# Optimization experiments

Hardware: AMD Instinct MI355X
Metric: run time of the kernel (lower is better)

## Reference

```python
import jax, jax.numpy as jnp
import numpy as np

VOCAB, EMB, H, NL = 50257, 1024, 2048, 2


def _lstm_cell(x, h, c, Wih, Whh, bih, bhh):
    # x: [1, in], h/c: [1, H]; PyTorch gate order i, f, g, o
    gates = x @ Wih.T + bih + h @ Whh.T + bhh  # [1, 4H]
    i, f, g, o = jnp.split(gates, 4, axis=-1)
    c2 = jax.nn.sigmoid(f) * c + jax.nn.sigmoid(i) * jnp.tanh(g)
    h2 = jax.nn.sigmoid(o) * jnp.tanh(c2)
    return h2, c2


def setup_inputs() -> dict:
    key = jax.random.key(0)
    ks = jax.random.split(key, 12)
    s = 0.02  # keep gate pre-activations in a sane range
    return {
        "input_ids": jax.random.randint(ks[0], (1,), 0, VOCAB, dtype=jnp.int64),
        "h0": jax.random.normal(ks[1], (2 * NL, 1, H), jnp.float32) * 0.1,
        "c0": jax.random.normal(ks[2], (2 * NL, 1, H), jnp.float32) * 0.1,
        "emb": jax.random.normal(ks[3], (VOCAB, EMB), jnp.float32),
        "W_ih_l0": jax.random.normal(ks[4], (2, 4 * H, EMB), jnp.float32) * s,
        "W_hh_l0": jax.random.normal(ks[5], (2, 4 * H, H), jnp.float32) * s,
        "b_ih_l0": jax.random.normal(ks[6], (2, 4 * H), jnp.float32) * s,
        "b_hh_l0": jax.random.normal(ks[7], (2, 4 * H), jnp.float32) * s,
        "W_ih_l1": jax.random.normal(ks[8], (2, 4 * H, 2 * H), jnp.float32) * s,
        "W_hh_l1": jax.random.normal(ks[9], (2, 4 * H, H), jnp.float32) * s,
        "b_ih_l1": jax.random.normal(ks[10], (2, 4 * H), jnp.float32) * s,
        "b_hh_l1": jax.random.normal(ks[11], (2, 4 * H), jnp.float32) * s,
    }


def reference(input_ids, h0, c0, emb, W_ih_l0, W_hh_l0, b_ih_l0, b_hh_l0,
              W_ih_l1, W_hh_l1, b_ih_l1, b_hh_l1):
    # embedded = embedding(input).view(1, 1, -1) -> seq_len=1, batch=1
    x = emb[input_ids]  # [1, EMB]
    layers = [(W_ih_l0, W_hh_l0, b_ih_l0, b_hh_l0),
              (W_ih_l1, W_hh_l1, b_ih_l1, b_hh_l1)]
    h_out, c_out = [], []
    for l, (Wih, Whh, bih, bhh) in enumerate(layers):
        # seq_len == 1: fwd and bwd directions both see the single timestep
        hf, cf = _lstm_cell(x, h0[2 * l], c0[2 * l], Wih[0], Whh[0], bih[0], bhh[0])
        hb, cb = _lstm_cell(x, h0[2 * l + 1], c0[2 * l + 1], Wih[1], Whh[1], bih[1], bhh[1])
        h_out += [hf, hb]
        c_out += [cf, cb]
        x = jnp.concatenate([hf, hb], axis=-1)  # [1, 2H] input to next layer
    output = x[None]  # [1, 1, 2H] (seq, batch, 2*hidden)
    h_n = jnp.stack(h_out, axis=0)  # [2*NL, 1, H]
    c_n = jnp.stack(c_out, axis=0)
    return output, h_n, c_n
```

## Files before the change

kernel.cpp:

```cpp
#include <hip/hip_runtime.h>


#define HID 2048
#define G4H 8192

__device__ __forceinline__ float wave_reduce_sum(float v) {
    #pragma unroll
    for (int off = 32; off > 0; off >>= 1)
        v += __shfl_down(v, off, 64);
    return v;
}
__device__ __forceinline__ float sigmoidf_(float v) { return 1.f / (1.f + expf(-v)); }

__global__ __launch_bounds__(256) void k1_gates0_part1(
    const int*   __restrict__ tok,
    const float* __restrict__ emb,
    const float* __restrict__ Wih0,
    const float* __restrict__ Whh0,
    const float* __restrict__ bih0,
    const float* __restrict__ bhh0,
    const float* __restrict__ Whh1,
    const float* __restrict__ bih1,
    const float* __restrict__ bhh1,
    const float* __restrict__ h0,
    float* __restrict__ gates0,
    float* __restrict__ part1)
{
    const int wave = (int)((blockIdx.x * blockDim.x + threadIdx.x) >> 6);
    const int lane = (int)(threadIdx.x & 63);

    if (wave < 2 * G4H) {
        const int dir = wave >> 13;
        const int r   = wave & (G4H - 1);
        const float*  x   = emb + (size_t)tok[0] * 1024;
        const float4* wih = (const float4*)(Wih0 + ((size_t)dir * G4H + r) * 1024);
        const float4* whh = (const float4*)(Whh0 + ((size_t)dir * G4H + r) * HID);
        const float4* xv  = (const float4*)x;
        const float4* hv  = (const float4*)(h0 + (size_t)dir * HID);

        float acc = 0.f;
        #pragma unroll
        for (int i = 0; i < 1024 / 4 / 64; ++i) {
            float4 w = wih[lane + i * 64], b = xv[lane + i * 64];
            acc += w.x * b.x + w.y * b.y + w.z * b.z + w.w * b.w;
        }
        #pragma unroll
        for (int i = 0; i < HID / 4 / 64; ++i) {
            float4 w = whh[lane + i * 64], b = hv[lane + i * 64];
            acc += w.x * b.x + w.y * b.y + w.z * b.z + w.w * b.w;
        }
        acc = wave_reduce_sum(acc);
        if (lane == 0) {
            int row = dir * G4H + r;
            gates0[row] = acc + bih0[row] + bhh0[row];
        }
    } else {
        const int w2  = wave - 2 * G4H;
        const int dir = w2 >> 13;
        const int r   = w2 & (G4H - 1);
        const float4* whh = (const float4*)(Whh1 + ((size_t)dir * G4H + r) * HID);
        const float4* hv  = (const float4*)(h0 + (size_t)(2 + dir) * HID);

        float acc = 0.f;
        #pragma unroll
        for (int i = 0; i < HID / 4 / 64; ++i) {
            float4 w = whh[lane + i * 64], b = hv[lane + i * 64];
            acc += w.x * b.x + w.y * b.y + w.z * b.z + w.w * b.w;
        }
        acc = wave_reduce_sum(acc);
        if (lane == 0) {
            int row = dir * G4H + r;
            part1[row] = acc + bih1[row] + bhh1[row];
        }
    }
}

__global__ __launch_bounds__(256) void k2_layer1(
    const float* __restrict__ gates0,
    const float* __restrict__ part1,
    const float* __restrict__ Wih1,
    const float* __restrict__ c0,
    float* __restrict__ out)
{
    __shared__ float x1[2 * HID];

    #pragma unroll
    for (int k = 0; k < 16; ++k) {
        const int idx = k * 256 + (int)threadIdx.x;
        const int dir = idx >> 11;
        const int j   = idx & (HID - 1);
        const float* g = gates0 + dir * G4H;
        float gi = g[j];
        float gf = g[HID + j];
        float gg = g[2 * HID + j];
        float go = g[3 * HID + j];
        float cp = c0[(size_t)dir * HID + j];
        float c2 = sigmoidf_(gf) * cp + sigmoidf_(gi) * tanhf(gg);
        float h2 = sigmoidf_(go) * tanhf(c2);
        x1[idx] = h2;
        if (blockIdx.x == 0) {
            out[4096  + (size_t)dir * HID + j] = h2;
            out[12288 + (size_t)dir * HID + j] = c2;
        }
    }
    __syncthreads();

    const int wave = (int)((blockIdx.x * blockDim.x + threadIdx.x) >> 6);
    const int lane = (int)(threadIdx.x & 63);
    const int dir  = wave >> 11;
    const int j    = wave & (HID - 1);

    const float4* xv = (const float4*)x1;
    float acc[4] = {0.f, 0.f, 0.f, 0.f};
    #pragma unroll
    for (int g = 0; g < 4; ++g) {
        const float4* wih = (const float4*)(Wih1 + ((size_t)dir * G4H + g * HID + j) * 4096);
        #pragma unroll 4
        for (int i = 0; i < 4096 / 4 / 64; ++i) {
            float4 w = wih[lane + i * 64], b = xv[lane + i * 64];
            acc[g] += w.x * b.x + w.y * b.y + w.z * b.z + w.w * b.w;
        }
    }
    #pragma unroll
    for (int g = 0; g < 4; ++g) acc[g] = wave_reduce_sum(acc[g]);

    if (lane == 0) {
        const int rb = dir * G4H + j;
        float gi = acc[0] + part1[rb];
        float gf = acc[1] + part1[rb + HID];
        float gg = acc[2] + part1[rb + 2 * HID];
        float go = acc[3] + part1[rb + 3 * HID];
        float cp = c0[(size_t)(2 + dir) * HID + j];
        float c2 = sigmoidf_(gf) * cp + sigmoidf_(gi) * tanhf(gg);
        float h2 = sigmoidf_(go) * tanhf(c2);
        out[4096  + (size_t)(2 + dir) * HID + j] = h2;
        out[12288 + (size_t)(2 + dir) * HID + j] = c2;
        out[(size_t)dir * HID + j] = h2;
    }
}

extern "C" void kernel_launch(void* const* d_in, const int* in_sizes, int n_in,
                              void* d_out, int out_size, void* d_ws, size_t ws_size,
                              hipStream_t stream) {
    const int*   ids  = (const int*)  d_in[0];
    const float* h0   = (const float*)d_in[1];
    const float* c0   = (const float*)d_in[2];
    const float* emb  = (const float*)d_in[3];
    const float* Wih0 = (const float*)d_in[4];
    const float* Whh0 = (const float*)d_in[5];
    const float* bih0 = (const float*)d_in[6];
    const float* bhh0 = (const float*)d_in[7];
    const float* Wih1 = (const float*)d_in[8];
    const float* Whh1 = (const float*)d_in[9];
    const float* bih1 = (const float*)d_in[10];
    const float* bhh1 = (const float*)d_in[11];

    float* out    = (float*)d_out;
    float* gates0 = (float*)d_ws;
    float* part1  = gates0 + 2 * G4H;

    k1_gates0_part1<<<8192, 256, 0, stream>>>(ids, emb, Wih0, Whh0, bih0, bhh0,
                                              Whh1, bih1, bhh1, h0, gates0, part1);
    k2_layer1<<<1024, 256, 0, stream>>>(gates0, part1, Wih1, c0, out);
}
```

Measured before the change: 116.9 us.

## Fuse layer-0 cell into gate GEMV kernel and split layer-1 gates across waves

The layer-0 LSTM cell nonlinearity moves into the first kernel. Each block now computes the four gate rows of one hidden unit in four waves, combines them through shared memory, and writes h/c directly. This removes the redundant per-block recomputation of the whole layer-0 cell (16 elements per thread in each of 1024 blocks) in the second kernel. The second kernel now uses 4096 blocks with one gate row per wave instead of four sequential rows per wave, which adds parallelism for the memory-bound Wih1 read. The cost is an extra __syncthreads per block and x1 being read from global memory rather than shared memory.

New measurement: 107.1 us. -8.4%, faster.

```diff
diff --git a/kernel.cpp b/kernel.cpp
--- a/kernel.cpp
+++ b/kernel.cpp
@@ -12,7 +12,19 @@
 }
 __device__ __forceinline__ float sigmoidf_(float v) { return 1.f / (1.f + expf(-v)); }
 
-__global__ __launch_bounds__(256) void k1_gates0_part1(
+__device__ __forceinline__ float dot_row(const float4* __restrict__ w,
+                                         const float4* __restrict__ v,
+                                         int lane, int n4) {
+    float acc = 0.f;
+    #pragma unroll 8
+    for (int i = 0; i < n4; ++i) {
+        float4 a = w[lane + i * 64], b = v[lane + i * 64];
+        acc += a.x * b.x + a.y * b.y + a.z * b.z + a.w * b.w;
+    }
+    return acc;
+}
+
+__global__ __launch_bounds__(256) void k1_l0cell_part1(
     const int*   __restrict__ tok,
     const float* __restrict__ emb,
     const float* __restrict__ Wih0,
@@ -23,113 +35,73 @@
     const float* __restrict__ bih1,
     const float* __restrict__ bhh1,
     const float* __restrict__ h0,
-    float* __restrict__ gates0,
+    const float* __restrict__ c0,
+    float* __restrict__ out,
+    float* __restrict__ x1,
     float* __restrict__ part1)
 {
-    const int wave = (int)((blockIdx.x * blockDim.x + threadIdx.x) >> 6);
     const int lane = (int)(threadIdx.x & 63);
+    const int w    = (int)(threadIdx.x >> 6);
+    const int bid  = (int)blockIdx.x;
 
-    if (wave < 2 * G4H) {
-        const int dir = wave >> 13;
-        const int r   = wave & (G4H - 1);
-        const float*  x   = emb + (size_t)tok[0] * 1024;
-        const float4* wih = (const float4*)(Wih0 + ((size_t)dir * G4H + r) * 1024);
-        const float4* whh = (const float4*)(Whh0 + ((size_t)dir * G4H + r) * HID);
-        const float4* xv  = (const float4*)x;
-        const float4* hv  = (const float4*)(h0 + (size_t)dir * HID);
+    if (bid < 4096) {
+        __shared__ float gsum[4];
+        const int dir = bid >> 11;
+        const int j   = bid & (HID - 1);
+        const int row = dir * G4H + w * HID + j;
 
-        float acc = 0.f;
-        #pragma unroll
-        for (int i = 0; i < 1024 / 4 / 64; ++i) {
-            float4 w = wih[lane + i * 64], b = xv[lane + i * 64];
-            acc += w.x * b.x + w.y * b.y + w.z * b.z + w.w * b.w;
-        }
-        #pragma unroll
-        for (int i = 0; i < HID / 4 / 64; ++i) {
-            float4 w = whh[lane + i * 64], b = hv[lane + i * 64];
-            acc += w.x * b.x + w.y * b.y + w.z * b.z + w.w * b.w;
-        }
+        const float* x = emb + (size_t)tok[0] * 1024;
+        float acc = dot_row((const float4*)(Wih0 + (size_t)row * 1024),
+                            (const float4*)x, lane, 1024 / 256);
+        acc += dot_row((const float4*)(Whh0 + (size_t)row * HID),
+                       (const float4*)(h0 + (size_t)dir * HID), lane, HID / 256);
         acc = wave_reduce_sum(acc);
-        if (lane == 0) {
-            int row = dir * G4H + r;
-            gates0[row] = acc + bih0[row] + bhh0[row];
+        if (lane == 0) gsum[w] = acc + bih0[row] + bhh0[row];
+        __syncthreads();
+        if (threadIdx.x == 0) {
+            float gi = gsum[0], gf = gsum[1], gg = gsum[2], go = gsum[3];
+            float cp = c0[(size_t)dir * HID + j];
+            float c2 = sigmoidf_(gf) * cp + sigmoidf_(gi) * tanhf(gg);
+            float h2 = sigmoidf_(go) * tanhf(c2);
+            x1[(size_t)dir * HID + j] = h2;
+            out[4096  + (size_t)dir * HID + j] = h2;
+            out[12288 + (size_t)dir * HID + j] = c2;
         }
     } else {
-        const int w2  = wave - 2 * G4H;
-        const int dir = w2 >> 13;
-        const int r   = w2 & (G4H - 1);
-        const float4* whh = (const float4*)(Whh1 + ((size_t)dir * G4H + r) * HID);
-        const float4* hv  = (const float4*)(h0 + (size_t)(2 + dir) * HID);
-
-        float acc = 0.f;
-        #pragma unroll
-        for (int i = 0; i < HID / 4 / 64; ++i) {
-            float4 w = whh[lane + i * 64], b = hv[lane + i * 64];
-            acc += w.x * b.x + w.y * b.y + w.z * b.z + w.w * b.w;
-        }
+        const int widx = (bid - 4096) * 4 + w;
+        const int dir  = widx >> 13;
+        const int r    = widx & (G4H - 1);
+        const int row  = dir * G4H + r;
+        float acc = dot_row((const float4*)(Whh1 + (size_t)row * HID),
+                            (const float4*)(h0 + (size_t)(2 + dir) * HID),
+                            lane, HID / 256);
         acc = wave_reduce_sum(acc);
-        if (lane == 0) {
-            int row = dir * G4H + r;
-            part1[row] = acc + bih1[row] + bhh1[row];
-        }
+        if (lane == 0) part1[row] = acc + bih1[row] + bhh1[row];
     }
 }
 
-__global__ __launch_bounds__(256) void k2_layer1(
-    const float* __restrict__ gates0,
+__global__ __launch_bounds__(256) void k2_l1cell(
+    const float* __restrict__ x1,
     const float* __restrict__ part1,
     const float* __restrict__ Wih1,
     const float* __restrict__ c0,
     float* __restrict__ out)
 {
-    __shared__ float x1[2 * HID];
+    __shared__ float gsum[4];
+    const int lane = (int)(threadIdx.x & 63);
+    const int w    = (int)(threadIdx.x >> 6);
+    const int bid  = (int)blockIdx.x;
+    const int dir  = bid >> 11;
+    const int j    = bid & (HID - 1);
+    const int row  = dir * G4H + w * HID + j;
 
-    #pragma unroll
-    for (int k = 0; k < 16; ++k) {
-        const int idx = k * 256 + (int)threadIdx.x;
-        const int dir = idx >> 11;
-        const int j   = idx & (HID - 1);
-        const float* g = gates0 + dir * G4H;
-        float gi = g[j];
-        float gf = g[HID + j];
-        float gg = g[2 * HID + j];
-        float go = g[3 * HID + j];
-        float cp = c0[(size_t)dir * HID + j];
-        float c2 = sigmoidf_(gf) * cp + sigmoidf_(gi) * tanhf(gg);
-        float h2 = sigmoidf_(go) * tanhf(c2);
-        x1[idx] = h2;
-        if (blockIdx.x == 0) {
-            out[4096  + (size_t)dir * HID + j] = h2;
-            out[12288 + (size_t)dir * HID + j] = c2;
-        }
-    }
+    float acc = dot_row((const float4*)(Wih1 + (size_t)row * 4096),
+                        (const float4*)x1, lane, 4096 / 256);
+    acc = wave_reduce_sum(acc);
+    if (lane == 0) gsum[w] = acc + part1[row];
     __syncthreads();
-
-    const int wave = (int)((blockIdx.x * blockDim.x + threadIdx.x) >> 6);
-    const int lane = (int)(threadIdx.x & 63);
-    const int dir  = wave >> 11;
-    const int j    = wave & (HID - 1);
-
-    const float4* xv = (const float4*)x1;
-    float acc[4] = {0.f, 0.f, 0.f, 0.f};
-    #pragma unroll
-    for (int g = 0; g < 4; ++g) {
-        const float4* wih = (const float4*)(Wih1 + ((size_t)dir * G4H + g * HID + j) * 4096);
-        #pragma unroll 4
-        for (int i = 0; i < 4096 / 4 / 64; ++i) {
-            float4 w = wih[lane + i * 64], b = xv[lane + i * 64];
-            acc[g] += w.x * b.x + w.y * b.y + w.z * b.z + w.w * b.w;
-        }
-    }
-    #pragma unroll
-    for (int g = 0; g < 4; ++g) acc[g] = wave_reduce_sum(acc[g]);
-
-    if (lane == 0) {
-        const int rb = dir * G4H + j;
-        float gi = acc[0] + part1[rb];
-        float gf = acc[1] + part1[rb + HID];
-        float gg = acc[2] + part1[rb + 2 * HID];
-        float go = acc[3] + part1[rb + 3 * HID];
+    if (threadIdx.x == 0) {
+        float gi = gsum[0], gf = gsum[1], gg = gsum[2], go = gsum[3];
         float cp = c0[(size_t)(2 + dir) * HID + j];
         float c2 = sigmoidf_(gf) * cp + sigmoidf_(gi) * tanhf(gg);
         float h2 = sigmoidf_(go) * tanhf(c2);
@@ -155,11 +127,12 @@
     const float* bih1 = (const float*)d_in[10];
     const float* bhh1 = (const float*)d_in[11];
 
-    float* out    = (float*)d_out;
-    float* gates0 = (float*)d_ws;
-    float* part1  = gates0 + 2 * G4H;
+    float* out   = (float*)d_out;
+    float* part1 = (float*)d_ws;
+    float* x1    = part1 + 2 * G4H;
 
-    k1_gates0_part1<<<8192, 256, 0, stream>>>(ids, emb, Wih0, Whh0, bih0, bhh0,
-                                              Whh1, bih1, bhh1, h0, gates0, part1);
-    k2_layer1<<<1024, 256, 0, stream>>>(gates0, part1, Wih1, c0, out);
+    k1_l0cell_part1<<<8192, 256, 0, stream>>>(ids, emb, Wih0, Whh0, bih0, bhh0,
+                                              Whh1, bih1, bhh1, h0, c0,
+                                              out, x1, part1);
+    k2_l1cell<<<4096, 256, 0, stream>>>(x1, part1, Wih1, c0, out);
 }
```
